# Performance work log

Measured on AMD Instinct MI355X. Metric: run time of the kernel, lower is better.

## Reference

```python
import jax, jax.numpy as jnp
import numpy as np

HEADS = 16
DIM_HEAD = 64
SCALE = DIM_HEAD ** -0.5
EPS = 1e-5


def _vdp_linear(mu, sigma, Wmu, Wsig_raw):
    # y = W x with W ~ N(Wmu, softplus(Wsig_raw)), x ~ N(mu, sigma) (diag covs):
    # Var(y) = (mu^2 + sigma) @ Wsig^T + sigma @ (Wmu^2)^T
    Wsig = jax.nn.softplus(Wsig_raw)
    mu_y = mu @ Wmu.T
    sigma_y = (mu * mu + sigma) @ Wsig.T + sigma @ (Wmu * Wmu).T
    return mu_y, sigma_y


def _vdp_layernorm(mu, sigma, gamma, beta):
    mean = jnp.mean(mu, axis=-1, keepdims=True)
    var = jnp.var(mu, axis=-1, keepdims=True)
    inv = 1.0 / jnp.sqrt(var + EPS)
    mu_y = (mu - mean) * inv * gamma + beta
    # first-order variance propagation through the affine normalization
    sigma_y = sigma * (gamma * gamma) * (inv * inv)
    return mu_y, sigma_y


def _vdp_softmax(mu, sigma):
    p = jax.nn.softmax(mu, axis=-1)
    # diagonal-Jacobian approximation: J_ii = p_i(1-p_i)
    J = p * (1.0 - p)
    return p, (J * J) * sigma


def setup_inputs() -> dict:
    key = jax.random.key(0)
    ks = jax.random.split(key, 6)
    B, N, D = 4, 1024, 1024
    inner = HEADS * DIM_HEAD  # 1024
    w_std = 0.02
    return {
        "mu": jax.random.normal(ks[0], (B, N, D), jnp.float32),
        "sigma": jax.random.uniform(ks[1], (B, N, D), jnp.float32),
        "ln_gamma": jnp.ones((D,), jnp.float32),
        "ln_beta": jnp.zeros((D,), jnp.float32),
        "Wqkv_mu": w_std * jax.random.normal(ks[2], (3 * inner, D), jnp.float32),
        "Wqkv_sigma_raw": -5.0 + 0.1 * jax.random.normal(ks[3], (3 * inner, D), jnp.float32),
        "Wout_mu": w_std * jax.random.normal(ks[4], (D, inner), jnp.float32),
        "Wout_sigma_raw": -5.0 + 0.1 * jax.random.normal(ks[5], (D, inner), jnp.float32),
    }


def reference(mu, sigma, ln_gamma, ln_beta, Wqkv_mu, Wqkv_sigma_raw, Wout_mu, Wout_sigma_raw):
    B, N, D = mu.shape

    mu_n, sigma_n = _vdp_layernorm(mu, sigma, ln_gamma, ln_beta)
    mu_qkv, sigma_qkv = _vdp_linear(mu_n, sigma_n, Wqkv_mu, Wqkv_sigma_raw)

    def split_heads(t):
        q, k, v = jnp.split(t, 3, axis=-1)
        rs = lambda a: a.reshape(B, N, HEADS, DIM_HEAD).transpose(0, 2, 1, 3)
        return rs(q), rs(k), rs(v)

    mu_q, mu_k, mu_v = split_heads(mu_qkv)
    sg_q, sg_k, sg_v = split_heads(sigma_qkv)

    mu_dots = jnp.einsum("bhid,bhjd->bhij", mu_q, mu_k) * SCALE
    sg_dots = jnp.einsum("bhid,bhjd->bhij", sg_q, sg_k) * SCALE

    mu_attn, sg_attn = _vdp_softmax(mu_dots, sg_dots)

    mu_o = jnp.einsum("bhij,bhjd->bhid", mu_attn, mu_v)
    sg_o = jnp.einsum("bhij,bhjd->bhid", sg_attn, sg_v)

    merge = lambda t: t.transpose(0, 2, 1, 3).reshape(B, N, HEADS * DIM_HEAD)
    mu_o, sg_o = merge(mu_o), merge(sg_o)

    return _vdp_linear(mu_o, sg_o, Wout_mu, Wout_sigma_raw)
```

## Files before the change

kernel.cpp:

```cpp
#include <hip/hip_runtime.h>

typedef unsigned short u16;
typedef unsigned int u32;
typedef __bf16 bf16x8 __attribute__((ext_vector_type(8)));
typedef float f32x4 __attribute__((ext_vector_type(4)));

__device__ __forceinline__ float b2f(u16 u) { return __uint_as_float(((u32)u) << 16); }
__device__ __forceinline__ u16 f2b(float f) {
  u32 u = __float_as_uint(f);
  u += 0x7fffu + ((u >> 16) & 1u);
  return (u16)(u >> 16);
}

__device__ __forceinline__ void gll16(const u16* g, u16* l) {
  __builtin_amdgcn_global_load_lds(
      (const __attribute__((address_space(1))) void*)g,
      (__attribute__((address_space(3))) void*)l, 16, 0, 0);
}

__device__ __forceinline__ float4 load4(const void* p, size_t idx, bool f32) {
  if (f32) return *(const float4*)((const float*)p + idx);
  ushort4 u = *(const ushort4*)((const u16*)p + idx);
  return make_float4(b2f(u.x), b2f(u.y), b2f(u.z), b2f(u.w));
}

__global__ __launch_bounds__(256) void detect_kernel(const u16* __restrict__ sig,
                                                     int* __restrict__ flag) {
  __shared__ int cnt;
  if (threadIdx.x == 0) cnt = 0;
  __syncthreads();
  int c = 0;
  for (int i = threadIdx.x; i < 65536; i += 256) {
    u16 v = sig[i];
    c += ((v & 0x7F80u) == 0x7F80u) ? 1 : 0;
  }
  atomicAdd(&cnt, c);
  __syncthreads();
  if (threadIdx.x == 0) *flag = (cnt >= 8) ? 1 : 0;
}

__device__ __forceinline__ float block_sum(float v, float* red, int t) {
  red[t] = v; __syncthreads();
  #pragma unroll
  for (int s = 128; s > 0; s >>= 1) {
    if (t < s) red[t] += red[t + s];
    __syncthreads();
  }
  float r = red[0];
  __syncthreads();
  return r;
}

__global__ __launch_bounds__(256) void ln_prep_kernel(
    const int* __restrict__ flag,
    const void* __restrict__ mu, const void* __restrict__ sigma,
    const void* __restrict__ gamma, const void* __restrict__ beta,
    u16* __restrict__ mu_n, u16* __restrict__ a1, u16* __restrict__ sgn)
{
  __shared__ float red[256];
  const bool f32 = (*flag != 0);
  const int t = threadIdx.x;
  const size_t base = (size_t)blockIdx.x * 1024 + (size_t)t * 4;
  float4 xm = load4(mu, base, f32);
  float4 xs = load4(sigma, base, f32);
  float x0 = xm.x, x1 = xm.y, x2 = xm.z, x3 = xm.w;
  float s0 = xs.x, s1 = xs.y, s2 = xs.z, s3 = xs.w;

  float sum = block_sum(x0 + x1 + x2 + x3, red, t);
  float ssq = block_sum(x0*x0 + x1*x1 + x2*x2 + x3*x3, red, t);
  float mean = sum * (1.0f / 1024.0f);
  float var  = ssq * (1.0f / 1024.0f) - mean * mean;
  float inv  = 1.0f / sqrtf(var + 1e-5f);
  float inv2 = inv * inv;

  float4 g4 = load4(gamma, (size_t)t * 4, f32);
  float4 b4 = load4(beta, (size_t)t * 4, f32);

  float m0 = (x0 - mean) * inv * g4.x + b4.x;
  float m1 = (x1 - mean) * inv * g4.y + b4.y;
  float m2 = (x2 - mean) * inv * g4.z + b4.z;
  float m3 = (x3 - mean) * inv * g4.w + b4.w;
  float v0 = s0 * g4.x * g4.x * inv2;
  float v1 = s1 * g4.y * g4.y * inv2;
  float v2 = s2 * g4.z * g4.z * inv2;
  float v3 = s3 * g4.w * g4.w * inv2;

  ushort4 omu = { f2b(m0), f2b(m1), f2b(m2), f2b(m3) };
  ushort4 oa1 = { f2b(m0*m0 + v0), f2b(m1*m1 + v1), f2b(m2*m2 + v2), f2b(m3*m3 + v3) };
  ushort4 osg = { f2b(v0), f2b(v1), f2b(v2), f2b(v3) };
  *(ushort4*)(mu_n + base) = omu;
  *(ushort4*)(a1 + base) = oa1;
  *(ushort4*)(sgn + base) = osg;
}

__global__ __launch_bounds__(256) void wprep_kernel(
    const int* __restrict__ flag,
    const void* __restrict__ wmu, const void* __restrict__ wsraw,
    u16* __restrict__ obf, u16* __restrict__ osig, u16* __restrict__ omsq, int n)
{
  const bool f32 = (*flag != 0);
  size_t idx = ((size_t)blockIdx.x * 256 + threadIdx.x) * 4;
  if (idx >= (size_t)n) return;
  float4 m4 = load4(wmu, idx, f32);
  float4 s4 = load4(wsraw, idx, f32);
  float m[4] = { m4.x, m4.y, m4.z, m4.w };
  float s[4] = { s4.x, s4.y, s4.z, s4.w };
  ushort4 ob, os, oq;
  u16* obp = (u16*)&ob; u16* osp = (u16*)&os; u16* oqp = (u16*)&oq;
  #pragma unroll
  for (int i = 0; i < 4; ++i) {
    float sp = (s[i] > 15.f) ? s[i] : log1pf(__expf(s[i]));
    obp[i] = f2b(m[i]);
    osp[i] = f2b(sp);
    oqp[i] = f2b(m[i] * m[i]);
  }
  *(ushort4*)(obf + idx) = ob;
  *(ushort4*)(osig + idx) = os;
  *(ushort4*)(omsq + idx) = oq;
}

template<bool DUAL, bool DYN>
__global__ __launch_bounds__(256) void gemm_bt_kernel(
    const u16* __restrict__ A0, const u16* __restrict__ B0,
    const u16* __restrict__ A1, const u16* __restrict__ B1,
    void* __restrict__ Cout, size_t obase, const int* __restrict__ flag,
    int M, int N, int K)
{
  __shared__ u16 lA[128 * 32];
  __shared__ u16 lB[128 * 32];
  const int t = threadIdx.x;
  const int n0 = blockIdx.x * 128, m0 = blockIdx.y * 128;
  const int lane = t & 63, wave = t >> 6;
  const int wr = (wave >> 1) * 64, wc = (wave & 1) * 64;
  const int ml = lane & 15, qd = lane >> 4;

  const int srow = t >> 2;
  const int scol = (t & 3) * 8;
  u16* lab = &lA[(size_t)wave * 512];
  u16* lbb = &lB[(size_t)wave * 512];

  f32x4 acc[4][4];
  #pragma unroll
  for (int i = 0; i < 4; ++i)
    #pragma unroll
    for (int j = 0; j < 4; ++j) acc[i][j] = (f32x4){0.f, 0.f, 0.f, 0.f};

  const int npair = DUAL ? 2 : 1;
  for (int pr = 0; pr < npair; ++pr) {
    const u16* A = pr ? A1 : A0;
    const u16* B = pr ? B1 : B0;
    for (int k0 = 0; k0 < K; k0 += 32) {
      __syncthreads();
      #pragma unroll
      for (int rep = 0; rep < 2; ++rep) {
        gll16(A + (size_t)(m0 + srow + rep * 64) * K + k0 + scol, lab + rep * 2048);
        gll16(B + (size_t)(n0 + srow + rep * 64) * K + k0 + scol, lbb + rep * 2048);
      }
      __syncthreads();
      bf16x8 af[4], bfr[4];
      #pragma unroll
      for (int ti = 0; ti < 4; ++ti)
        af[ti] = *(const bf16x8*)&lA[(wr + ti * 16 + ml) * 32 + qd * 8];
      #pragma unroll
      for (int tj = 0; tj < 4; ++tj)
        bfr[tj] = *(const bf16x8*)&lB[(wc + tj * 16 + ml) * 32 + qd * 8];
      #pragma unroll
      for (int ti = 0; ti < 4; ++ti)
        #pragma unroll
        for (int tj = 0; tj < 4; ++tj)
          acc[ti][tj] = __builtin_amdgcn_mfma_f32_16x16x32_bf16(af[ti], bfr[tj], acc[ti][tj], 0, 0, 0);
    }
  }

  const bool of32 = DYN && (*flag != 0);
  #pragma unroll
  for (int ti = 0; ti < 4; ++ti) {
    int row = m0 + wr + ti * 16 + qd * 4;
    #pragma unroll
    for (int tj = 0; tj < 4; ++tj) {
      int col = n0 + wc + tj * 16 + ml;
      #pragma unroll
      for (int r = 0; r < 4; ++r) {
        float v = acc[ti][tj][r];
        size_t off = obase + (size_t)(row + r) * N + col;
        if (DYN) {
          if (of32) ((float*)Cout)[off] = v;
          else      ((u16*)Cout)[off] = f2b(v);
        } else {
          ((u16*)Cout)[off] = f2b(v);
        }
      }
    }
  }
}

__global__ __launch_bounds__(512, 4) void attn_kernel(
    const u16* __restrict__ qkv_mu, const u16* __restrict__ qkv_sg,
    u16* __restrict__ o_mu, u16* __restrict__ a1o, u16* __restrict__ o_sg)
{
  __shared__ u16 lKW[128 * 72];
  __shared__ u16 lV[128 * 72];
  __shared__ u16 lP[128 * 72];

  const int t = threadIdx.x;
  const int wv = t >> 6, lane = t & 63;
  const int ml = lane & 15, qd = lane >> 4;
  const int b = blockIdx.y >> 4, h = blockIdx.y & 15;
  const size_t rowbase = (size_t)b * 1024 * 3072;
  const int i0 = blockIdx.x * 128;
  const int qcol = h * 64, kcol = 1024 + h * 64, vcol = 2048 + h * 64;
  const int qrow = wv * 16;

  bf16x8 aQm[2], aQs[2];
  #pragma unroll
  for (int ks = 0; ks < 2; ++ks) {
    size_t ga = rowbase + (size_t)(i0 + qrow + ml) * 3072 + qcol + ks * 32 + qd * 8;
    aQm[ks] = *(const bf16x8*)(qkv_mu + ga);
    aQs[ks] = *(const bf16x8*)(qkv_sg + ga);
  }

  float mfin[4], lacc[4];
  #pragma unroll
  for (int r = 0; r < 4; ++r) { mfin[r] = -1e30f; lacc[r] = 0.f; }

  for (int j0 = 0; j0 < 1024; j0 += 128) {
    __syncthreads();
    #pragma unroll
    for (int rep = 0; rep < 2; ++rep) {
      int c = t + rep * 512;
      int row = c >> 3, seg = c & 7;
      *(uint4*)&lKW[row * 72 + seg * 8] =
          *(const uint4*)(qkv_mu + rowbase + (size_t)(j0 + row) * 3072 + kcol + seg * 8);
    }
    __syncthreads();
    f32x4 s8[8];
    #pragma unroll
    for (int tj = 0; tj < 8; ++tj) {
      bf16x8 b0 = *(const bf16x8*)&lKW[(tj * 16 + ml) * 72 + qd * 8];
      bf16x8 b1 = *(const bf16x8*)&lKW[(tj * 16 + ml) * 72 + 32 + qd * 8];
      f32x4 s = (f32x4){0.f, 0.f, 0.f, 0.f};
      s = __builtin_amdgcn_mfma_f32_16x16x32_bf16(aQm[0], b0, s, 0, 0, 0);
      s = __builtin_amdgcn_mfma_f32_16x16x32_bf16(aQm[1], b1, s, 0, 0, 0);
      s8[tj] = s;
    }
    #pragma unroll
    for (int r = 0; r < 4; ++r) {
      float nm = mfin[r];
      #pragma unroll
      for (int tj = 0; tj < 8; ++tj) nm = fmaxf(nm, s8[tj][r] * 0.125f);
      float add = 0.f;
      #pragma unroll
      for (int tj = 0; tj < 8; ++tj) add += __expf(s8[tj][r] * 0.125f - nm);
      lacc[r] = lacc[r] * __expf(mfin[r] - nm) + add;
      mfin[r] = nm;
    }
  }
  #pragma unroll
  for (int r = 0; r < 4; ++r) {
    float m = mfin[r], l = lacc[r];
    #pragma unroll
    for (int xo = 1; xo < 16; xo <<= 1) {
      float om = __shfl_xor(m, xo, 64);
      float ol = __shfl_xor(l, xo, 64);
      float nm = fmaxf(m, om);
      l = l * __expf(m - nm) + ol * __expf(om - nm);
      m = nm;
    }
    mfin[r] = m;
    lacc[r] = 1.0f / l;
  }

  f32x4 accm[4], accs[4];
  #pragma unroll
  for (int tj = 0; tj < 4; ++tj) {
    accm[tj] = (f32x4){0.f, 0.f, 0.f, 0.f};
    accs[tj] = (f32x4){0.f, 0.f, 0.f, 0.f};
  }

  for (int j0 = 0; j0 < 1024; j0 += 64) {
    __syncthreads();
    #pragma unroll
    for (int rep = 0; rep < 2; ++rep) {
      int c = t + rep * 512;
      int row = c >> 3, seg = c & 7;
      const u16* src = (row < 64) ? qkv_mu : qkv_sg;
      int rr = row & 63;
      *(uint4*)&lKW[row * 72 + seg * 8] =
          *(const uint4*)(src + rowbase + (size_t)(j0 + rr) * 3072 + kcol + seg * 8);
    }
    {
      int buf = t >> 8, rem = t & 255;
      int db = rem >> 4, tb = rem & 15;
      const u16* src = buf ? qkv_sg : qkv_mu;
      ushort4 vals[4];
      #pragma unroll
      for (int i = 0; i < 4; ++i)
        vals[i] = *(const ushort4*)(src + rowbase + (size_t)(j0 + tb * 4 + i) * 3072 + vcol + db * 4);
      #pragma unroll
      for (int k = 0; k < 4; ++k) {
        ushort4 o;
        u16* op = (u16*)&o;
        const u16* v0 = (const u16*)&vals[0];
        const u16* v1 = (const u16*)&vals[1];
        const u16* v2 = (const u16*)&vals[2];
        const u16* v3 = (const u16*)&vals[3];
        op[0] = v0[k]; op[1] = v1[k]; op[2] = v2[k]; op[3] = v3[k];
        *(ushort4*)&lV[(buf * 64 + db * 4 + k) * 72 + tb * 4] = o;
      }
    }
    __syncthreads();

    f32x4 sm[4], ss[4];
    #pragma unroll
    for (int tj = 0; tj < 4; ++tj) {
      bf16x8 bm0 = *(const bf16x8*)&lKW[(tj * 16 + ml) * 72 + qd * 8];
      bf16x8 bm1 = *(const bf16x8*)&lKW[(tj * 16 + ml) * 72 + 32 + qd * 8];
      bf16x8 bs0 = *(const bf16x8*)&lKW[(64 + tj * 16 + ml) * 72 + qd * 8];
      bf16x8 bs1 = *(const bf16x8*)&lKW[(64 + tj * 16 + ml) * 72 + 32 + qd * 8];
      f32x4 s = (f32x4){0.f, 0.f, 0.f, 0.f};
      s = __builtin_amdgcn_mfma_f32_16x16x32_bf16(aQm[0], bm0, s, 0, 0, 0);
      s = __builtin_amdgcn_mfma_f32_16x16x32_bf16(aQm[1], bm1, s, 0, 0, 0);
      sm[tj] = s;
      f32x4 s2 = (f32x4){0.f, 0.f, 0.f, 0.f};
      s2 = __builtin_amdgcn_mfma_f32_16x16x32_bf16(aQs[0], bs0, s2, 0, 0, 0);
      s2 = __builtin_amdgcn_mfma_f32_16x16x32_bf16(aQs[1], bs1, s2, 0, 0, 0);
      ss[tj] = s2;
    }
    __syncthreads();

    #pragma unroll
    for (int tj = 0; tj < 4; ++tj)
      #pragma unroll
      for (int r = 0; r < 4; ++r) {
        float p = __expf(sm[tj][r] * 0.125f - mfin[r]) * lacc[r];
        float jp = p * (1.0f - p);
        float w = jp * jp * (ss[tj][r] * 0.125f);
        int row = qrow + qd * 4 + r;
        lP[row * 72 + tj * 16 + ml]  = f2b(p);
        lKW[row * 72 + tj * 16 + ml] = f2b(w);
      }
    __syncthreads();

    bf16x8 ap[2], aw[2];
    #pragma unroll
    for (int ks = 0; ks < 2; ++ks) {
      ap[ks] = *(const bf16x8*)&lP[(qrow + ml) * 72 + ks * 32 + qd * 8];
      aw[ks] = *(const bf16x8*)&lKW[(qrow + ml) * 72 + ks * 32 + qd * 8];
    }
    #pragma unroll
    for (int tj = 0; tj < 4; ++tj) {
      bf16x8 vm0 = *(const bf16x8*)&lV[(tj * 16 + ml) * 72 + qd * 8];
      bf16x8 vm1 = *(const bf16x8*)&lV[(tj * 16 + ml) * 72 + 32 + qd * 8];
      bf16x8 vs0 = *(const bf16x8*)&lV[(64 + tj * 16 + ml) * 72 + qd * 8];
      bf16x8 vs1 = *(const bf16x8*)&lV[(64 + tj * 16 + ml) * 72 + 32 + qd * 8];
      accm[tj] = __builtin_amdgcn_mfma_f32_16x16x32_bf16(ap[0], vm0, accm[tj], 0, 0, 0);
      accm[tj] = __builtin_amdgcn_mfma_f32_16x16x32_bf16(ap[1], vm1, accm[tj], 0, 0, 0);
      accs[tj] = __builtin_amdgcn_mfma_f32_16x16x32_bf16(aw[0], vs0, accs[tj], 0, 0, 0);
      accs[tj] = __builtin_amdgcn_mfma_f32_16x16x32_bf16(aw[1], vs1, accs[tj], 0, 0, 0);
    }
  }

  #pragma unroll
  for (int tj = 0; tj < 4; ++tj)
    #pragma unroll
    for (int r = 0; r < 4; ++r) {
      int row = i0 + qrow + qd * 4 + r;
      size_t off = ((size_t)b * 1024 + row) * 1024 + h * 64 + tj * 16 + ml;
      float om = accm[tj][r], os = accs[tj][r];
      o_mu[off] = f2b(om);
      a1o[off]  = f2b(fmaf(om, om, os));
      o_sg[off] = f2b(os);
    }
}

extern "C" void kernel_launch(void* const* d_in, const int* in_sizes, int n_in,
                              void* d_out, int out_size, void* d_ws, size_t ws_size,
                              hipStream_t stream)
{
  (void)in_sizes; (void)n_in; (void)out_size; (void)ws_size;
  const void* mu        = d_in[0];
  const void* sigma     = d_in[1];
  const void* gamma     = d_in[2];
  const void* beta      = d_in[3];
  const void* wqkv_mu   = d_in[4];
  const void* wqkv_sraw = d_in[5];
  const void* wout_mu   = d_in[6];
  const void* wout_sraw = d_in[7];

  u16* ws = (u16*)d_ws;
  const size_t R = 4096;
  u16* mu_n   = ws;
  u16* a1     = mu_n + R * 1024;
  u16* sgn    = a1 + R * 1024;
  u16* wq_bf  = sgn + R * 1024;
  u16* wq_sig = wq_bf + 3072 * 1024;
  u16* wq_msq = wq_sig + 3072 * 1024;
  u16* wo_bf  = wq_msq + 3072 * 1024;
  u16* wo_sig = wo_bf + 1024 * 1024;
  u16* wo_msq = wo_sig + 1024 * 1024;
  u16* mu_qkv = wo_msq + 1024 * 1024;
  u16* sg_qkv = mu_qkv + R * 3072;
  int* flag   = (int*)(sg_qkv + R * 3072);

  u16* mu_o = mu_n;
  u16* a1o  = a1;
  u16* sgo  = sgn;

  detect_kernel<<<1, 256, 0, stream>>>((const u16*)sigma, flag);
  ln_prep_kernel<<<4096, 256, 0, stream>>>(flag, mu, sigma, gamma, beta, mu_n, a1, sgn);
  wprep_kernel<<<(3072 * 1024) / 1024, 256, 0, stream>>>(flag, wqkv_mu, wqkv_sraw,
                                                         wq_bf, wq_sig, wq_msq, 3072 * 1024);
  wprep_kernel<<<(1024 * 1024) / 1024, 256, 0, stream>>>(flag, wout_mu, wout_sraw,
                                                         wo_bf, wo_sig, wo_msq, 1024 * 1024);

  gemm_bt_kernel<false, false><<<dim3(24, 32), 256, 0, stream>>>(
      mu_n, wq_bf, nullptr, nullptr, mu_qkv, 0, nullptr, 4096, 3072, 1024);
  gemm_bt_kernel<true, false><<<dim3(24, 32), 256, 0, stream>>>(
      a1, wq_sig, sgn, wq_msq, sg_qkv, 0, nullptr, 4096, 3072, 1024);

  attn_kernel<<<dim3(8, 64), 512, 0, stream>>>(mu_qkv, sg_qkv, mu_o, a1o, sgo);

  gemm_bt_kernel<false, true><<<dim3(8, 32), 256, 0, stream>>>(
      mu_o, wo_bf, nullptr, nullptr, d_out, 0, flag, 4096, 1024, 1024);
  gemm_bt_kernel<true, true><<<dim3(8, 32), 256, 0, stream>>>(
      a1o, wo_sig, sgo, wo_msq, d_out, (size_t)R * 1024, flag, 4096, 1024, 1024);
}
```

Baseline: 448.3 us.

## Interleave variance operands into K=2048 rows and merge mean/variance GEMMs into one launch

New measurement: 442.8 us. No clear change (-1.2%).

```diff
diff --git a/kernel.cpp b/kernel.cpp
--- a/kernel.cpp
+++ b/kernel.cpp
@@ -55,7 +55,7 @@
     const int* __restrict__ flag,
     const void* __restrict__ mu, const void* __restrict__ sigma,
     const void* __restrict__ gamma, const void* __restrict__ beta,
-    u16* __restrict__ mu_n, u16* __restrict__ a1, u16* __restrict__ sgn)
+    u16* __restrict__ mu_n, u16* __restrict__ a1sg)
 {
   __shared__ float red[256];
   const bool f32 = (*flag != 0);
@@ -89,18 +89,20 @@
   ushort4 oa1 = { f2b(m0*m0 + v0), f2b(m1*m1 + v1), f2b(m2*m2 + v2), f2b(m3*m3 + v3) };
   ushort4 osg = { f2b(v0), f2b(v1), f2b(v2), f2b(v3) };
   *(ushort4*)(mu_n + base) = omu;
-  *(ushort4*)(a1 + base) = oa1;
-  *(ushort4*)(sgn + base) = osg;
+  size_t r2 = (size_t)blockIdx.x * 2048 + (size_t)t * 4;
+  *(ushort4*)(a1sg + r2) = oa1;
+  *(ushort4*)(a1sg + r2 + 1024) = osg;
 }
 
 __global__ __launch_bounds__(256) void wprep_kernel(
     const int* __restrict__ flag,
     const void* __restrict__ wmu, const void* __restrict__ wsraw,
-    u16* __restrict__ obf, u16* __restrict__ osig, u16* __restrict__ omsq, int n)
+    u16* __restrict__ obf, u16* __restrict__ os2, int n)
 {
   const bool f32 = (*flag != 0);
   size_t idx = ((size_t)blockIdx.x * 256 + threadIdx.x) * 4;
   if (idx >= (size_t)n) return;
+  int row = (int)(idx >> 10), k = (int)(idx & 1023);
   float4 m4 = load4(wmu, idx, f32);
   float4 s4 = load4(wsraw, idx, f32);
   float m[4] = { m4.x, m4.y, m4.z, m4.w };
@@ -115,29 +117,33 @@
     oqp[i] = f2b(m[i] * m[i]);
   }
   *(ushort4*)(obf + idx) = ob;
-  *(ushort4*)(osig + idx) = os;
-  *(ushort4*)(omsq + idx) = oq;
-}
-
-template<bool DUAL, bool DYN>
-__global__ __launch_bounds__(256) void gemm_bt_kernel(
-    const u16* __restrict__ A0, const u16* __restrict__ B0,
-    const u16* __restrict__ A1, const u16* __restrict__ B1,
-    void* __restrict__ Cout, size_t obase, const int* __restrict__ flag,
-    int M, int N, int K)
+  size_t r2 = (size_t)row * 2048 + k;
+  *(ushort4*)(os2 + r2) = os;
+  *(ushort4*)(os2 + r2 + 1024) = oq;
+}
+
+template<bool DYN>
+__global__ __launch_bounds__(256) void gemm_pair_kernel(
+    const u16* __restrict__ A0, const u16* __restrict__ B0, int K0, void* C0, size_t ob0,
+    const u16* __restrict__ A1, const u16* __restrict__ B1, int K1, void* C1, size_t ob1,
+    int split, int N, const int* __restrict__ flag)
 {
-  __shared__ u16 lA[128 * 32];
-  __shared__ u16 lB[128 * 32];
+  __shared__ u16 lA[128 * 64];
+  __shared__ u16 lB[128 * 64];
   const int t = threadIdx.x;
-  const int n0 = blockIdx.x * 128, m0 = blockIdx.y * 128;
+  int bx = blockIdx.x;
+  const u16 *A, *B; void* C; size_t obase; int K;
+  if (bx < split) { A = A0; B = B0; K = K0; C = C0; obase = ob0; }
+  else { bx -= split; A = A1; B = B1; K = K1; C = C1; obase = ob1; }
+
+  const int n0 = bx * 128, m0 = blockIdx.y * 128;
   const int lane = t & 63, wave = t >> 6;
   const int wr = (wave >> 1) * 64, wc = (wave & 1) * 64;
   const int ml = lane & 15, qd = lane >> 4;
 
-  const int srow = t >> 2;
-  const int scol = (t & 3) * 8;
-  u16* lab = &lA[(size_t)wave * 512];
-  u16* lbb = &lB[(size_t)wave * 512];
+  const int srow = t >> 3;
+  const int gseg = (t & 7) ^ (srow & 7);
+  const int mlx = ml & 7;
 
   f32x4 acc[4][4];
   #pragma unroll
@@ -145,25 +151,25 @@
     #pragma unroll
     for (int j = 0; j < 4; ++j) acc[i][j] = (f32x4){0.f, 0.f, 0.f, 0.f};
 
-  const int npair = DUAL ? 2 : 1;
-  for (int pr = 0; pr < npair; ++pr) {
-    const u16* A = pr ? A1 : A0;
-    const u16* B = pr ? B1 : B0;
-    for (int k0 = 0; k0 < K; k0 += 32) {
-      __syncthreads();
-      #pragma unroll
-      for (int rep = 0; rep < 2; ++rep) {
-        gll16(A + (size_t)(m0 + srow + rep * 64) * K + k0 + scol, lab + rep * 2048);
-        gll16(B + (size_t)(n0 + srow + rep * 64) * K + k0 + scol, lbb + rep * 2048);
-      }
-      __syncthreads();
+  for (int k0 = 0; k0 < K; k0 += 64) {
+    __syncthreads();
+    #pragma unroll
+    for (int rep = 0; rep < 4; ++rep) {
+      gll16(A + (size_t)(m0 + srow + rep * 32) * K + k0 + gseg * 8,
+            lA + rep * 2048 + wave * 512);
+      gll16(B + (size_t)(n0 + srow + rep * 32) * K + k0 + gseg * 8,
+            lB + rep * 2048 + wave * 512);
+    }
+    __syncthreads();
+    #pragma unroll
+    for (int kk = 0; kk < 2; ++kk) {
       bf16x8 af[4], bfr[4];
       #pragma unroll
       for (int ti = 0; ti < 4; ++ti)
-        af[ti] = *(const bf16x8*)&lA[(wr + ti * 16 + ml) * 32 + qd * 8];
+        af[ti] = *(const bf16x8*)&lA[(wr + ti * 16 + ml) * 64 + (((kk * 4 + qd) ^ mlx)) * 8];
       #pragma unroll
       for (int tj = 0; tj < 4; ++tj)
-        bfr[tj] = *(const bf16x8*)&lB[(wc + tj * 16 + ml) * 32 + qd * 8];
+        bfr[tj] = *(const bf16x8*)&lB[(wc + tj * 16 + ml) * 64 + (((kk * 4 + qd) ^ mlx)) * 8];
       #pragma unroll
       for (int ti = 0; ti < 4; ++ti)
         #pragma unroll
@@ -184,10 +190,10 @@
         float v = acc[ti][tj][r];
         size_t off = obase + (size_t)(row + r) * N + col;
         if (DYN) {
-          if (of32) ((float*)Cout)[off] = v;
-          else      ((u16*)Cout)[off] = f2b(v);
+          if (of32) ((float*)C)[off] = v;
+          else      ((u16*)C)[off] = f2b(v);
         } else {
-          ((u16*)Cout)[off] = f2b(v);
+          ((u16*)C)[off] = f2b(v);
         }
       }
     }
@@ -196,7 +202,7 @@
 
 __global__ __launch_bounds__(512, 4) void attn_kernel(
     const u16* __restrict__ qkv_mu, const u16* __restrict__ qkv_sg,
-    u16* __restrict__ o_mu, u16* __restrict__ a1o, u16* __restrict__ o_sg)
+    u16* __restrict__ o_mu, u16* __restrict__ a1sgo)
 {
   __shared__ u16 lKW[128 * 72];
   __shared__ u16 lV[128 * 72];
@@ -365,11 +371,13 @@
     #pragma unroll
     for (int r = 0; r < 4; ++r) {
       int row = i0 + qrow + qd * 4 + r;
-      size_t off = ((size_t)b * 1024 + row) * 1024 + h * 64 + tj * 16 + ml;
+      int col = h * 64 + tj * 16 + ml;
+      size_t rowg = (size_t)b * 1024 + row;
       float om = accm[tj][r], os = accs[tj][r];
-      o_mu[off] = f2b(om);
-      a1o[off]  = f2b(fmaf(om, om, os));
-      o_sg[off] = f2b(os);
+      o_mu[rowg * 1024 + col] = f2b(om);
+      size_t r2 = rowg * 2048 + col;
+      a1sgo[r2] = f2b(fmaf(om, om, os));
+      a1sgo[r2 + 1024] = f2b(os);
     }
 }
 
@@ -390,38 +398,34 @@
   u16* ws = (u16*)d_ws;
   const size_t R = 4096;
   u16* mu_n   = ws;
-  u16* a1     = mu_n + R * 1024;
-  u16* sgn    = a1 + R * 1024;
-  u16* wq_bf  = sgn + R * 1024;
-  u16* wq_sig = wq_bf + 3072 * 1024;
-  u16* wq_msq = wq_sig + 3072 * 1024;
-  u16* wo_bf  = wq_msq + 3072 * 1024;
-  u16* wo_sig = wo_bf + 1024 * 1024;
-  u16* wo_msq = wo_sig + 1024 * 1024;
-  u16* mu_qkv = wo_msq + 1024 * 1024;
+  u16* a1sg   = mu_n + R * 1024;
+  u16* wq_bf  = a1sg + R * 2048;
+  u16* wqs2   = wq_bf + 3072 * 1024;
+  u16* wo_bf  = wqs2 + 3072 * 2048;
+  u16* wos2   = wo_bf + 1024 * 1024;
+  u16* mu_qkv = wos2 + 1024 * 2048;
   u16* sg_qkv = mu_qkv + R * 3072;
   int* flag   = (int*)(sg_qkv + R * 3072);
 
-  u16* mu_o = mu_n;
-  u16* a1o  = a1;
-  u16* sgo  = sgn;
+  u16* mu_o  = mu_n;
+  u16* a1sgo = a1sg;
 
   detect_kernel<<<1, 256, 0, stream>>>((const u16*)sigma, flag);
-  ln_prep_kernel<<<4096, 256, 0, stream>>>(flag, mu, sigma, gamma, beta, mu_n, a1, sgn);
+  ln_prep_kernel<<<4096, 256, 0, stream>>>(flag, mu, sigma, gamma, beta, mu_n, a1sg);
   wprep_kernel<<<(3072 * 1024) / 1024, 256, 0, stream>>>(flag, wqkv_mu, wqkv_sraw,
-                                                         wq_bf, wq_sig, wq_msq, 3072 * 1024);
+                                                         wq_bf, wqs2, 3072 * 1024);
   wprep_kernel<<<(1024 * 1024) / 1024, 256, 0, stream>>>(flag, wout_mu, wout_sraw,
-                                                         wo_bf, wo_sig, wo_msq, 1024 * 1024);
-
-  gemm_bt_kernel<false, false><<<dim3(24, 32), 256, 0, stream>>>(
-      mu_n, wq_bf, nullptr, nullptr, mu_qkv, 0, nullptr, 4096, 3072, 1024);
-  gemm_bt_kernel<true, false><<<dim3(24, 32), 256, 0, stream>>>(
-      a1, wq_sig, sgn, wq_msq, sg_qkv, 0, nullptr, 4096, 3072, 1024);
-
-  attn_kernel<<<dim3(8, 64), 512, 0, stream>>>(mu_qkv, sg_qkv, mu_o, a1o, sgo);
-
-  gemm_bt_kernel<false, true><<<dim3(8, 32), 256, 0, stream>>>(
-      mu_o, wo_bf, nullptr, nullptr, d_out, 0, flag, 4096, 1024, 1024);
-  gemm_bt_kernel<true, true><<<dim3(8, 32), 256, 0, stream>>>(
-      a1o, wo_sig, sgo, wo_msq, d_out, (size_t)R * 1024, flag, 4096, 1024, 1024);
-}
+                                                         wo_bf, wos2, 1024 * 1024);
+
+  gemm_pair_kernel<false><<<dim3(48, 32), 256, 0, stream>>>(
+      mu_n, wq_bf, 1024, mu_qkv, 0,
+      a1sg, wqs2, 2048, sg_qkv, 0,
+      24, 3072, nullptr);
+
+  attn_kernel<<<dim3(8, 64), 512, 0, stream>>>(mu_qkv, sg_qkv, mu_o, a1sgo);
+
+  gemm_pair_kernel<true><<<dim3(16, 32), 256, 0, stream>>>(
+      mu_o, wo_bf, 1024, d_out, 0,
+      a1sgo, wos2, 2048, d_out, R * 1024,
+      8, 1024, flag);
+}
```
